# Kernel optimization log

Measured on AMD Instinct MI355X. Metric: run time of the kernel, lower is better.

## Reference

```python
import jax, jax.numpy as jnp
import numpy as np

E, D, I, TOPK, N = 8, 2048, 4096, 2, 4096


def setup_inputs() -> dict:
    key = jax.random.key(0)
    k_x, k_w, k_i, k_g, k_u, k_d = jax.random.split(key, 6)
    x = jax.random.normal(k_x, (N, D), dtype=jnp.float32)
    expert_weights = jax.random.uniform(k_w, (N, TOPK), dtype=jnp.float32)
    expert_indices = jax.random.randint(k_i, (N, TOPK), 0, E).astype(jnp.int32)
    s_in = np.float32(1.0 / np.sqrt(D))
    s_mid = np.float32(1.0 / np.sqrt(I))
    # SwitchLinear weights: [num_experts, out_features, in_features]
    wg = jax.random.normal(k_g, (E, I, D), dtype=jnp.float32) * s_in
    wu = jax.random.normal(k_u, (E, I, D), dtype=jnp.float32) * s_in
    wd = jax.random.normal(k_d, (E, D, I), dtype=jnp.float32) * s_mid
    return {"x": x, "expert_weights": expert_weights,
            "expert_indices": expert_indices, "top_k": TOPK,
            "wg": wg, "wu": wu, "wd": wd}


def reference(x, expert_weights, expert_indices, top_k, wg, wu, wd):
    # out[n] = sum_k expert_weights[n,k] * Wd[e] @ (silu(Wg[e] x[n]) * (Wu[e] x[n]))
    #          with e = expert_indices[n,k].
    # Grouped-by-expert form (identical math): accumulate each expert's
    # contribution over all tokens, weighted by its routing weight (0 if not routed).
    num_experts = wg.shape[0]
    out = jnp.zeros_like(x)
    for e in range(num_experts):
        # per-token routing weight for expert e (sums over top_k slots)
        w_e = jnp.sum(jnp.where(expert_indices == e, expert_weights, 0.0), axis=-1)  # [N]
        gate = x @ wg[e].T            # [N, I]
        up = x @ wu[e].T              # [N, I]
        h = jax.nn.silu(gate) * up    # SwiGLU, [N, I]
        out = out + w_e[:, None] * (h @ wd[e].T)  # [N, D]
    return out
```

## Files before the change

kernel.cpp:

```cpp
#include <hip/hip_runtime.h>
#include <hip/hip_bf16.h>
#include <math.h>

#define E_ 8
#define D_ 2048
#define I_ 4096
#define TOPK_ 2
#define N_ 4096
#define NPAIR (N_*TOPK_)
#define PADMAX 10240
#define MAXTB 40
#define CVTX 12
#define CH_X   (1L<<20)
#define CH_HALF (1L<<22)
#define CH_WD  (1L<<23)

typedef __attribute__((ext_vector_type(8))) short s8v;
typedef __attribute__((ext_vector_type(8))) unsigned short us8;
typedef __attribute__((ext_vector_type(4))) float f32x4;
typedef const __attribute__((address_space(1))) void* gvp;
typedef __attribute__((address_space(3))) void* lvp;

__device__ __forceinline__ unsigned short f2bf(float f) {
  union { float f; unsigned int u; } c; c.f = f;
  unsigned int u = c.u;
  u += 0x7fffu + ((u >> 16) & 1u);
  return (unsigned short)(u >> 16);
}

__device__ __forceinline__ void cvt_chunk(const float* __restrict__ src,
                                          unsigned short* __restrict__ dst,
                                          size_t off) {
  float4 a = *(const float4*)(src + off);
  float4 b = *(const float4*)(src + off + 4);
  us8 o;
  o[0]=f2bf(a.x); o[1]=f2bf(a.y); o[2]=f2bf(a.z); o[3]=f2bf(a.w);
  o[4]=f2bf(b.x); o[5]=f2bf(b.y); o[6]=f2bf(b.z); o[7]=f2bf(b.w);
  *(us8*)(dst + off) = o;
}

__device__ __forceinline__ void cvt_half(const float* __restrict__ src,
                                         unsigned short* __restrict__ dst,
                                         long chunk, int ihalf) {
  long f = chunk << 3;
  int e = (int)(f >> 22);
  long r = f & ((1L << 22) - 1);
  size_t off = ((size_t)e << 23) + ((size_t)ihalf << 22) + (size_t)r;
  cvt_chunk(src, dst, off);
}

__global__ __launch_bounds__(512)
void head_kernel(const int* __restrict__ idx, const float* __restrict__ ew,
                 int* cnt, int* offs, int* tb, int* ntb,
                 int* perm, float* wgt,
                 const float* __restrict__ x, unsigned short* __restrict__ xb,
                 const float* __restrict__ wg, unsigned short* __restrict__ wgb,
                 const float* __restrict__ wu, unsigned short* __restrict__ wub)
{
  if (blockIdx.x == 0) {
    __shared__ int scnt[E_], soff[E_ + 1], scur[E_];
    int t = threadIdx.x;
    if (t < E_) scnt[t] = 0;
    __syncthreads();
    for (int p = t; p < NPAIR; p += blockDim.x) atomicAdd(&scnt[idx[p]], 1);
    __syncthreads();
    if (t == 0) {
      int o = 0;
      for (int e = 0; e < E_; e++) {
        soff[e] = o; scur[e] = o;
        o += ((scnt[e] + 255) / 256) * 256;
      }
      soff[E_] = o;
      int T = 0;
      for (int e = 0; e < E_; e++) {
        int nb = (scnt[e] + 255) / 256;
        for (int rb = 0; rb < nb; rb++) tb[T++] = (e << 16) | rb;
      }
      *ntb = T;
      for (int e = 0; e < E_; e++) { cnt[e] = scnt[e]; offs[e] = soff[e]; }
      offs[E_] = o;
    }
    __syncthreads();
    for (int e = 0; e < E_; e++) {
      int start = soff[e] + scnt[e], end = soff[e + 1];
      for (int s = start + t; s < end; s += blockDim.x) { perm[s] = -1; wgt[s] = 0.f; }
    }
    __syncthreads();
    for (int p = t; p < NPAIR; p += blockDim.x) {
      int e = idx[p];
      int pos = atomicAdd(&scur[e], 1);
      perm[pos] = p / TOPK_;
      wgt[pos]  = ew[p];
    }
    return;
  }
  const long TOTAL = CH_X + 2 * CH_HALF;
  long c0 = (long)(blockIdx.x - 1) * 512 + threadIdx.x;
  long stride = (long)(gridDim.x - 1) * 512;
  for (long c = c0; c < TOTAL; c += stride) {
    if (c < CH_X) cvt_chunk(x, xb, (size_t)c << 3);
    else if (c < CH_X + CH_HALF) cvt_half(wg, wgb, c - CH_X, 0);
    else cvt_half(wu, wub, c - CH_X - CH_HALF, 0);
  }
}


#define SB  __builtin_amdgcn_sched_barrier(0)
#define BARR __builtin_amdgcn_s_barrier()
#define VMW(N) asm volatile("s_waitcnt vmcnt(" #N ")" ::: "memory")
#define PRIO1 __builtin_amdgcn_s_setprio(1)
#define PRIO0 __builtin_amdgcn_s_setprio(0)

#define STG(T,P) { \
  __builtin_amdgcn_global_load_lds((gvp)(aptr + (size_t)(T)*32), (lvp)(&smem[(P)*8192 + w*512]), 16, 0, 0); \
  __builtin_amdgcn_global_load_lds((gvp)(bptr + (size_t)(T)*32), (lvp)(&smem[16384 + (P)*8192 + w*512]), 16, 0, 0); }

#define TILE32(T,P,NT_) { \
  if ((T) == (NT_)-1) { VMW(0); } else { VMW(2); } \
  SB; BARR; SB; \
  { const unsigned short* ap_ = &smem[(P)*8192 + aOff]; \
    const unsigned short* bp_ = &smem[16384 + (P)*8192 + bOff]; \
    s8v af[4], bf[4]; \
    af[0]=*(const s8v*)(ap_);      af[1]=*(const s8v*)(ap_+512); \
    af[2]=*(const s8v*)(ap_+1024); af[3]=*(const s8v*)(ap_+1536); \
    bf[0]=*(const s8v*)(bp_);      bf[1]=*(const s8v*)(bp_+512); \
    bf[2]=*(const s8v*)(bp_+1024); bf[3]=*(const s8v*)(bp_+1536); \
    PRIO1; \
    _Pragma("unroll") for (int m_=0;m_<4;m_++) \
      _Pragma("unroll") for (int n_=0;n_<4;n_++) \
        acc[m_][n_] = __builtin_amdgcn_mfma_f32_16x16x32_bf16(af[m_], bf[n_], acc[m_][n_], 0,0,0); \
    PRIO0; } \
  SB; BARR; SB; \
  if ((T)+2 < (NT_)) { STG((T)+2, P); } }

#define KLOOP32(NT_) { \
  STG(0,0); STG(1,1); \
  _Pragma("unroll 1") for (int tt=0; tt<(NT_)/2; ++tt) { \
    TILE32(2*tt,   0, NT_); \
    TILE32(2*tt+1, 1, NT_); } }

__global__ __launch_bounds__(1024, 4)
void gu32_kernel(const unsigned short* __restrict__ xb,
                 const unsigned short* __restrict__ wgb,
                 const unsigned short* __restrict__ wub,
                 const int* __restrict__ tb, const int* __restrict__ ntb,
                 const int* __restrict__ offs, const int* __restrict__ perm,
                 unsigned short* __restrict__ H,
                 int i_base, int cvt_mode,
                 const float* __restrict__ cs0, unsigned short* __restrict__ cd0,
                 const float* __restrict__ cs1, unsigned short* __restrict__ cd1)
{
  __shared__ unsigned short smem[32768];

  int tid = threadIdx.x;
  if (blockIdx.x >= MAXTB) {
    long cid = (long)(blockIdx.x - MAXTB) + (long)CVTX * blockIdx.y;
    long c0 = cid * 1024 + tid;
    long stride = (long)CVTX * 16 * 1024;
    if (cvt_mode == 1) {
      for (long c = c0; c < 2 * CH_HALF; c += stride) {
        if (c < CH_HALF) cvt_half(cs0, cd0, c, 1);
        else cvt_half(cs1, cd1, c - CH_HALF, 1);
      }
    } else if (cvt_mode == 2) {
      for (long c = c0; c < CH_WD; c += stride) cvt_chunk(cs0, cd0, (size_t)c << 3);
    }
    return;
  }

  int lid = blockIdx.y * MAXTB + blockIdx.x;
  int sid = (lid & 7) * (MAXTB * 16 / 8) + (lid >> 3);
  int bx = sid % MAXTB;
  int by = sid / MAXTB;
  if (bx >= *ntb) return;
  int ent = tb[bx];
  int e = ent >> 16, rb = ent & 0xffff;
  int slotbase = offs[e] + rb * 256;
  int i0 = i_base + by * 128;

  int lane = tid & 63, w = tid >> 6;
  int wr = w >> 2, wc = w & 3;

  int cS = (lane & 7) ^ (lane >> 3);
  int rrS = 2 * (lane >> 3) + (cS >> 2);
  int kcS = (cS & 3) * 8;
  int tok = perm[slotbase + w * 16 + rrS]; if (tok < 0) tok = 0;
  const unsigned short* aptr = xb + (size_t)tok * D_ + kcS;
  const unsigned short* bptr = ((w & 1) ? wub : wgb)
      + ((size_t)e * I_ + i0 + (w >> 1) * 16 + rrS) * D_ + kcS;

  int hl = (lane & 15) >> 1;
  int pA = (((lane & 1) * 4 + (lane >> 4)) ^ hl) * 8;
  int aOff = wr * 2048 + hl * 64 + pA;
  int bOff = wc * 2048 + hl * 64 + pA;

  f32x4 acc[4][4];
#pragma unroll
  for (int m = 0; m < 4; m++)
#pragma unroll
    for (int n = 0; n < 4; n++) acc[m][n] = f32x4{0.f,0.f,0.f,0.f};

  KLOOP32(64);

#pragma unroll
  for (int m = 0; m < 4; m++) {
#pragma unroll
    for (int r = 0; r < 4; r++) {
      int row = wr * 64 + m * 16 + (lane >> 4) * 4 + r;
      size_t hbase = (size_t)(slotbase + row) * I_ + i0 + (lane & 15);
#pragma unroll
      for (int pr = 0; pr < 2; pr++) {
        float g = acc[m][pr*2][r];
        float u = acc[m][pr*2+1][r];
        float h = (g / (1.0f + __expf(-g))) * u;
        H[hbase + (2 * wc + pr) * 16] = f2bf(h);
      }
    }
  }
}

__global__ __launch_bounds__(1024, 4)
void down32_kernel(const unsigned short* __restrict__ H,
                   const unsigned short* __restrict__ wdb,
                   const int* __restrict__ tb, const int* __restrict__ ntb,
                   const int* __restrict__ offs, const int* __restrict__ perm,
                   const float* __restrict__ wgt,
                   float* __restrict__ out)
{
  __shared__ unsigned short smem[32768];

  int tid = threadIdx.x;
  int lid = blockIdx.y * MAXTB + blockIdx.x;
  int sid = (lid & 7) * (MAXTB * 8 / 8) + (lid >> 3);
  int bx = sid % MAXTB;
  int by = sid / MAXTB;
  if (bx >= *ntb) return;
  int ent = tb[bx];
  int e = ent >> 16, rb = ent & 0xffff;
  int slotbase = offs[e] + rb * 256;
  int d0 = by * 256;

  int lane = tid & 63, w = tid >> 6;
  int wr = w >> 2, wc = w & 3;

  int cS = (lane & 7) ^ (lane >> 3);
  int rrS = 2 * (lane >> 3) + (cS >> 2);
  int kcS = (cS & 3) * 8;
  const unsigned short* aptr = H + (size_t)(slotbase + w * 16 + rrS) * I_ + kcS;
  const unsigned short* bptr = wdb + ((size_t)e * D_ + d0 + w * 16 + rrS) * I_ + kcS;

  int hl = (lane & 15) >> 1;
  int pA = (((lane & 1) * 4 + (lane >> 4)) ^ hl) * 8;
  int aOff = wr * 2048 + hl * 64 + pA;
  int bOff = wc * 2048 + hl * 64 + pA;

  f32x4 acc[4][4];
#pragma unroll
  for (int m = 0; m < 4; m++)
#pragma unroll
    for (int n = 0; n < 4; n++) acc[m][n] = f32x4{0.f,0.f,0.f,0.f};

  KLOOP32(128);

#pragma unroll
  for (int m = 0; m < 4; m++) {
#pragma unroll
    for (int r = 0; r < 4; r++) {
      int row = wr * 64 + m * 16 + (lane >> 4) * 4 + r;
      int s = slotbase + row;
      int tok = perm[s];
      if (tok < 0) continue;
      float wv = wgt[s];
      float* op = out + (size_t)tok * D_ + d0 + wc * 64 + (lane & 15);
#pragma unroll
      for (int n = 0; n < 4; n++)
        atomicAdd(op + n * 16, acc[m][n][r] * wv);
    }
  }
}

extern "C" void kernel_launch(void* const* d_in, const int* in_sizes, int n_in,
                              void* d_out, int out_size, void* d_ws, size_t ws_size,
                              hipStream_t stream)
{
  const float* x  = (const float*)d_in[0];
  const float* ew = (const float*)d_in[1];
  const int*  idx = (const int*)d_in[2];
  const float* wg = (const float*)d_in[4];
  const float* wu = (const float*)d_in[5];
  const float* wd = (const float*)d_in[6];
  float* out = (float*)d_out;

  char* ws = (char*)d_ws;
  int* cnt   = (int*)(ws);
  int* ntb   = (int*)(ws + 64);
  int* tb    = (int*)(ws + 128);
  int* offs  = (int*)(ws + 640);
  int* perm  = (int*)(ws + 4096);
  float* wgt = (float*)(ws + 4096 + PADMAX * 4);

  const size_t xb_off = 131072;
  const size_t xb_b   = (size_t)N_ * D_ * 2;
  const size_t H_b    = (size_t)PADMAX * I_ * 2;
  const size_t w_b    = (size_t)E_ * I_ * D_ * 2;
  unsigned short* xb  = (unsigned short*)(ws + xb_off);
  unsigned short* H   = (unsigned short*)(ws + xb_off + xb_b);
  unsigned short* wgb = (unsigned short*)(ws + xb_off + xb_b + H_b);
  unsigned short* wub = (unsigned short*)((char*)wgb + w_b);
  unsigned short* wdb = (unsigned short*)((char*)wub + w_b);

  hipMemsetAsync(d_out, 0, (size_t)N_ * D_ * sizeof(float), stream);
  head_kernel<<<2048, 512, 0, stream>>>(idx, ew, cnt, offs, tb, ntb, perm, wgt,
                                        x, xb, wg, wgb, wu, wub);
  gu32_kernel<<<dim3(MAXTB + CVTX, 16), 1024, 0, stream>>>(
      xb, wgb, wub, tb, ntb, offs, perm, H, 0, 1, wg, wgb, wu, wub);
  gu32_kernel<<<dim3(MAXTB + CVTX, 16), 1024, 0, stream>>>(
      xb, wgb, wub, tb, ntb, offs, perm, H, I_ / 2, 2, wd, wdb,
      (const float*)0, (unsigned short*)0);
  down32_kernel<<<dim3(MAXTB, 8), 1024, 0, stream>>>(
      H, wdb, tb, ntb, offs, perm, wgt, out);
}
```

Before: 815.4 us.

## Convert full gate/up weights in head and merge gate-up launches into one

The head kernel now converts all of wg and wu to bf16 up front, no longer just the first half of the intermediate dimension. The two half-width gate/up GEMM launches collapse into one launch over the full intermediate range, whose spare blocks convert wd concurrently. This removes one kernel launch and the split overlap schedule, but the head kernel's serial conversion work doubles before any GEMM can start.

```diff
diff --git a/kernel.cpp b/kernel.cpp
--- a/kernel.cpp
+++ b/kernel.cpp
@@ -10,9 +10,9 @@
 #define NPAIR (N_*TOPK_)
 #define PADMAX 10240
 #define MAXTB 40
-#define CVTX 12
+#define CVTX 24
 #define CH_X   (1L<<20)
-#define CH_HALF (1L<<22)
+#define CH_FULL (1L<<23)
 #define CH_WD  (1L<<23)
 
 typedef __attribute__((ext_vector_type(8))) short s8v;
@@ -37,16 +37,6 @@
   o[0]=f2bf(a.x); o[1]=f2bf(a.y); o[2]=f2bf(a.z); o[3]=f2bf(a.w);
   o[4]=f2bf(b.x); o[5]=f2bf(b.y); o[6]=f2bf(b.z); o[7]=f2bf(b.w);
   *(us8*)(dst + off) = o;
-}
-
-__device__ __forceinline__ void cvt_half(const float* __restrict__ src,
-                                         unsigned short* __restrict__ dst,
-                                         long chunk, int ihalf) {
-  long f = chunk << 3;
-  int e = (int)(f >> 22);
-  long r = f & ((1L << 22) - 1);
-  size_t off = ((size_t)e << 23) + ((size_t)ihalf << 22) + (size_t)r;
-  cvt_chunk(src, dst, off);
 }
 
 __global__ __launch_bounds__(512)
@@ -94,13 +84,13 @@
     }
     return;
   }
-  const long TOTAL = CH_X + 2 * CH_HALF;
+  const long TOTAL = CH_X + 2 * CH_FULL;
   long c0 = (long)(blockIdx.x - 1) * 512 + threadIdx.x;
   long stride = (long)(gridDim.x - 1) * 512;
   for (long c = c0; c < TOTAL; c += stride) {
     if (c < CH_X) cvt_chunk(x, xb, (size_t)c << 3);
-    else if (c < CH_X + CH_HALF) cvt_half(wg, wgb, c - CH_X, 0);
-    else cvt_half(wu, wub, c - CH_X - CH_HALF, 0);
+    else if (c < CH_X + CH_FULL) cvt_chunk(wg, wgb, (size_t)(c - CH_X) << 3);
+    else cvt_chunk(wu, wub, (size_t)(c - CH_X - CH_FULL) << 3);
   }
 }
 
@@ -146,9 +136,7 @@
                  const int* __restrict__ tb, const int* __restrict__ ntb,
                  const int* __restrict__ offs, const int* __restrict__ perm,
                  unsigned short* __restrict__ H,
-                 int i_base, int cvt_mode,
-                 const float* __restrict__ cs0, unsigned short* __restrict__ cd0,
-                 const float* __restrict__ cs1, unsigned short* __restrict__ cd1)
+                 const float* __restrict__ wd, unsigned short* __restrict__ wdb)
 {
   __shared__ unsigned short smem[32768];
 
@@ -156,27 +144,20 @@
   if (blockIdx.x >= MAXTB) {
     long cid = (long)(blockIdx.x - MAXTB) + (long)CVTX * blockIdx.y;
     long c0 = cid * 1024 + tid;
-    long stride = (long)CVTX * 16 * 1024;
-    if (cvt_mode == 1) {
-      for (long c = c0; c < 2 * CH_HALF; c += stride) {
-        if (c < CH_HALF) cvt_half(cs0, cd0, c, 1);
-        else cvt_half(cs1, cd1, c - CH_HALF, 1);
-      }
-    } else if (cvt_mode == 2) {
-      for (long c = c0; c < CH_WD; c += stride) cvt_chunk(cs0, cd0, (size_t)c << 3);
-    }
+    long stride = (long)CVTX * 32 * 1024;
+    for (long c = c0; c < CH_WD; c += stride) cvt_chunk(wd, wdb, (size_t)c << 3);
     return;
   }
 
   int lid = blockIdx.y * MAXTB + blockIdx.x;
-  int sid = (lid & 7) * (MAXTB * 16 / 8) + (lid >> 3);
+  int sid = (lid & 7) * (MAXTB * 32 / 8) + (lid >> 3);
   int bx = sid % MAXTB;
   int by = sid / MAXTB;
   if (bx >= *ntb) return;
   int ent = tb[bx];
   int e = ent >> 16, rb = ent & 0xffff;
   int slotbase = offs[e] + rb * 256;
-  int i0 = i_base + by * 128;
+  int i0 = by * 128;
 
   int lane = tid & 63, w = tid >> 6;
   int wr = w >> 2, wc = w & 3;
@@ -312,11 +293,8 @@
   hipMemsetAsync(d_out, 0, (size_t)N_ * D_ * sizeof(float), stream);
   head_kernel<<<2048, 512, 0, stream>>>(idx, ew, cnt, offs, tb, ntb, perm, wgt,
                                         x, xb, wg, wgb, wu, wub);
-  gu32_kernel<<<dim3(MAXTB + CVTX, 16), 1024, 0, stream>>>(
-      xb, wgb, wub, tb, ntb, offs, perm, H, 0, 1, wg, wgb, wu, wub);
-  gu32_kernel<<<dim3(MAXTB + CVTX, 16), 1024, 0, stream>>>(
-      xb, wgb, wub, tb, ntb, offs, perm, H, I_ / 2, 2, wd, wdb,
-      (const float*)0, (unsigned short*)0);
+  gu32_kernel<<<dim3(MAXTB + CVTX, 32), 1024, 0, stream>>>(
+      xb, wgb, wub, tb, ntb, offs, perm, H, wd, wdb);
   down32_kernel<<<dim3(MAXTB, 8), 1024, 0, stream>>>(
       H, wdb, tb, ntb, offs, perm, wgt, out);
 }
```

Result: slower. 927.0 us (+13.7%).
